# Performance work log

Measured on AMD Instinct MI355X. Metric: run time of the kernel, lower is better.

The kernel has to match this reference:

```python
import jax, jax.numpy as jnp
import numpy as np

B = 8          # batch of images
FH = FW = 28   # feature map size (layer2 of wide_resnet101_2 on 224x224)
IMG = 224      # input image H=W
C = 1024       # embedding dim (max of layer2/layer3 channels)
M = 50000      # coreset memory bank size
KS = 17        # GaussianBlur kernel size
SIGMA = 4.0


def _gauss_kernel():
    x = jnp.arange(KS, dtype=jnp.float32) - (KS - 1) / 2.0
    g = jnp.exp(-(x * x) / (2.0 * SIGMA * SIGMA))
    return g / jnp.sum(g)


def _gaussian_blur(masks):
    # masks: [B, H, W]; separable depthwise blur with reflect padding
    k = _gauss_kernel()
    pad = (KS - 1) // 2
    x = jnp.pad(masks, ((0, 0), (pad, pad), (pad, pad)), mode='reflect')[:, None]  # [B,1,H+2p,W+2p]
    x = jax.lax.conv_general_dilated(x, k[None, None, :, None], (1, 1), 'VALID',
                                     dimension_numbers=('NCHW', 'OIHW', 'NCHW'))
    x = jax.lax.conv_general_dilated(x, k[None, None, None, :], (1, 1), 'VALID',
                                     dimension_numbers=('NCHW', 'OIHW', 'NCHW'))
    return x[:, 0]


def setup_inputs() -> dict:
    key = jax.random.key(0)
    k1, k2 = jax.random.split(key)
    features = jax.random.normal(k1, (B * FH * FW, C), dtype=jnp.float32)
    memory = jax.random.normal(k2, (M, C), dtype=jnp.float32)
    return {"features": features, "memory": memory}


def reference(features, memory):
    # pairwise squared L2 distances via ||f||^2 + ||m||^2 - 2 f.m  -> [N, M]
    f2 = jnp.sum(features * features, axis=-1)            # [N]
    m2 = jnp.sum(memory * memory, axis=-1)                # [M]
    d2 = f2[:, None] + m2[None, :] - 2.0 * (features @ memory.T)
    score = jnp.sqrt(jnp.maximum(jnp.min(d2, axis=-1), 0.0))  # [N]
    image_scores = jnp.max(score.reshape(B, -1), axis=-1)     # [B]
    masks = score.reshape(B, FH, FW)
    # bilinear, align_corners=False == jax.image.resize 'linear' (half-pixel centers)
    masks = jax.image.resize(masks, (B, IMG, IMG), method='linear')
    masks = _gaussian_blur(masks)
    return image_scores, masks
```

## Files before the change

kernel.cpp:

```cpp
#include <hip/hip_runtime.h>
#include <hip/hip_bf16.h>
#include <float.h>

#define N_FEAT 6272
#define N_FPAD 6400
#define C_DIM  1024
#define M_MEM  50000
#define M_PAD  50176
#define B_IMG  8
#define IMGSZ  224
#define NTM    25
#define NTN    196
#define NT     4900

typedef __attribute__((ext_vector_type(8))) short bf16x8;
typedef __attribute__((ext_vector_type(4))) float f32x4;


__device__ inline unsigned short f2bf(float x) {
  unsigned int u = __float_as_uint(x);
  u += 0x7FFFu + ((u >> 16) & 1u);
  return (unsigned short)(u >> 16);
}

__global__ __launch_bounds__(256) void convert_rows_kernel(
    const float* __restrict__ src, unsigned short* __restrict__ dst,
    float* __restrict__ sq, unsigned int* __restrict__ minbits,
    int valid_rows, int total_rows)
{
  int row  = blockIdx.x * 4 + (threadIdx.x >> 6);
  int lane = threadIdx.x & 63;
  if (row >= total_rows) return;
  float s = 0.f;
  ushort4* d4 = (ushort4*)(dst + (size_t)row * C_DIM);
  if (row < valid_rows) {
    const float4* s4 = (const float4*)(src + (size_t)row * C_DIM);
    #pragma unroll
    for (int j = 0; j < 4; ++j) {
      float4 v = s4[lane + 64 * j];
      ushort4 o = make_ushort4(f2bf(v.x), f2bf(v.y), f2bf(v.z), f2bf(v.w));
      d4[lane + 64 * j] = o;
      s += v.x * v.x + v.y * v.y + v.z * v.z + v.w * v.w;
    }
  } else {
    ushort4 z = make_ushort4(0, 0, 0, 0);
    #pragma unroll
    for (int j = 0; j < 4; ++j) d4[lane + 64 * j] = z;
  }
  #pragma unroll
  for (int off = 32; off > 0; off >>= 1) s += __shfl_down(s, off, 64);
  if (lane == 0) {
    sq[row] = (row < valid_rows) ? s : FLT_MAX;
    if (minbits && row < valid_rows) minbits[row] = 0x7F7FFFFFu;
  }
}

__global__ __launch_bounds__(512, 2) void gemm_min_kernel(
    const unsigned short* __restrict__ A,
    const unsigned short* __restrict__ Bm,
    const float* __restrict__ f2, const float* __restrict__ m2,
    unsigned int* __restrict__ minbits)
{
  extern __shared__ char smem[];

  const int orig = blockIdx.x;
  const int xcd  = orig & 7;
  const int wg   = ((xcd < 4) ? xcd * 613 : 2452 + (xcd - 4) * 612) + (orig >> 3);
  const int g    = wg / 980;
  const int rem  = wg - g * 980;
  const int tileN = rem / 5;
  const int tileM = g * 5 + (rem - tileN * 5);

  const int tid  = threadIdx.x;
  const int w    = tid >> 6, lane = tid & 63;
  const int wr   = w >> 2, wc = w & 3;
  const int quad = lane >> 4, r16 = lane & 15;

  const unsigned short* gAp[2];
  const unsigned short* gBp[2];
  int offA[2], offB[2];
  {
    const int rowInBlk = lane >> 2;
    const int qsrc = (lane & 3) ^ ((lane >> 3) & 3);
    #pragma unroll
    for (int j = 0; j < 2; ++j) {
      const int m = w * 2 + j;
      const int row = m * 16 + rowInBlk;
      gAp[j] = A  + (size_t)(tileM * 256 + row) * C_DIM + qsrc * 8;
      gBp[j] = Bm + (size_t)(tileN * 256 + row) * C_DIM + qsrc * 8;
      offA[j] = m * 1024;
      offB[j] = 16384 + m * 1024;
    }
  }

  auto stage = [&](int kt) {
    char* sl = smem + ((kt & 3) << 15);
    const int ko = kt * 32;
    #pragma unroll
    for (int j = 0; j < 2; ++j) {
      __builtin_amdgcn_global_load_lds(
        (const __attribute__((address_space(1))) unsigned int*)(gAp[j] + ko),
        (__attribute__((address_space(3))) unsigned int*)(sl + offA[j]), 16, 0, 0);
      __builtin_amdgcn_global_load_lds(
        (const __attribute__((address_space(1))) unsigned int*)(gBp[j] + ko),
        (__attribute__((address_space(3))) unsigned int*)(sl + offB[j]), 16, 0, 0);
    }
  };

  f32x4 acc[8][4] = {};
  const int fsw   = quad ^ ((r16 >> 1) & 3);
  const int aBase = (wr * 128 + r16) * 4 + fsw;
  const int bBase = (wc * 64  + r16) * 4 + fsw;

  stage(0); stage(1); stage(2);

  auto body = [&](int kt, bool doStage) {
    __builtin_amdgcn_s_barrier();
    __builtin_amdgcn_sched_barrier(0);
    if (doStage) stage(kt + 3);
    const char* base = smem + ((kt & 3) << 15);
    const bf16x8* LA = (const bf16x8*)base;
    const bf16x8* LB = (const bf16x8*)(base + 16384);
    bf16x8 b[4], a[4];
    #pragma unroll
    for (int j = 0; j < 4; ++j) b[j] = LB[bBase + j * 64];
    #pragma unroll
    for (int i = 0; i < 4; ++i) a[i] = LA[aBase + i * 64];
    __builtin_amdgcn_s_setprio(1);
    #pragma unroll
    for (int i = 0; i < 4; ++i)
      #pragma unroll
      for (int j = 0; j < 4; ++j)
        acc[i][j] = __builtin_amdgcn_mfma_f32_16x16x32_bf16(a[i], b[j], acc[i][j], 0, 0, 0);
    __builtin_amdgcn_s_setprio(0);
    bf16x8 a2[4];
    #pragma unroll
    for (int i = 0; i < 4; ++i) a2[i] = LA[aBase + (i + 4) * 64];
    __builtin_amdgcn_s_barrier();
    __builtin_amdgcn_sched_barrier(0);
    __builtin_amdgcn_s_setprio(1);
    #pragma unroll
    for (int i = 0; i < 4; ++i)
      #pragma unroll
      for (int j = 0; j < 4; ++j)
        acc[i + 4][j] = __builtin_amdgcn_mfma_f32_16x16x32_bf16(a2[i], b[j], acc[i + 4][j], 0, 0, 0);
    __builtin_amdgcn_s_setprio(0);
  };

  for (int kt = 0; kt < 30; ++kt) {
    asm volatile("s_waitcnt vmcnt(8)" ::: "memory");
    body(kt, kt < 29);
  }
  asm volatile("s_waitcnt vmcnt(4)" ::: "memory");
  body(30, false);
  asm volatile("s_waitcnt vmcnt(0)" ::: "memory");
  body(31, false);

  const int colbase = tileN * 256 + wc * 64 + r16;
  float m2v[4];
  #pragma unroll
  for (int j = 0; j < 4; ++j) m2v[j] = m2[colbase + j * 16];
  const int rowq = tileM * 256 + wr * 128 + quad * 4;
  #pragma unroll
  for (int i = 0; i < 8; ++i) {
    #pragma unroll
    for (int r = 0; r < 4; ++r) {
      const int n = rowq + i * 16 + r;
      const float f2v = f2[n];
      float best = FLT_MAX;
      #pragma unroll
      for (int j = 0; j < 4; ++j) {
        float d = f2v + m2v[j] - 2.0f * acc[i][j][r];
        d = fmaxf(d, 0.0f);
        best = fminf(best, d);
      }
      best = fminf(best, __shfl_xor(best, 1, 64));
      best = fminf(best, __shfl_xor(best, 2, 64));
      best = fminf(best, __shfl_xor(best, 4, 64));
      best = fminf(best, __shfl_xor(best, 8, 64));
      if (r16 == 0) atomicMin(minbits + n, __float_as_uint(best));
    }
  }
}

__global__ __launch_bounds__(256) void finalize_kernel(
    const unsigned int* __restrict__ minbits, float* __restrict__ m28,
    float* __restrict__ image_scores)
{
  int b = blockIdx.x, tid = threadIdx.x;
  float mx = 0.f;
  for (int i = tid; i < 784; i += 256) {
    float s = sqrtf(__uint_as_float(minbits[b * 784 + i]));
    m28[b * 784 + i] = s;
    mx = fmaxf(mx, s);
  }
  #pragma unroll
  for (int off = 32; off > 0; off >>= 1) mx = fmaxf(mx, __shfl_down(mx, off, 64));
  __shared__ float red[4];
  if ((tid & 63) == 0) red[tid >> 6] = mx;
  __syncthreads();
  if (tid == 0) image_scores[b] = fmaxf(fmaxf(red[0], red[1]), fmaxf(red[2], red[3]));
}

__global__ __launch_bounds__(256) void resize_kernel(
    const float* __restrict__ m28, float* __restrict__ out)
{
  int idx = blockIdx.x * 256 + threadIdx.x;
  if (idx >= B_IMG * IMGSZ * IMGSZ) return;
  int x = idx % IMGSZ, y = (idx / IMGSZ) % IMGSZ, b = idx / (IMGSZ * IMGSZ);
  float sy = (y + 0.5f) * 0.125f - 0.5f;
  float sx = (x + 0.5f) * 0.125f - 0.5f;
  int iy0 = (int)floorf(sy); float fy = sy - (float)iy0;
  int ix0 = (int)floorf(sx); float fx = sx - (float)ix0;
  int y0 = min(max(iy0, 0), 27), y1 = min(max(iy0 + 1, 0), 27);
  int x0 = min(max(ix0, 0), 27), x1 = min(max(ix0 + 1, 0), 27);
  const float* p = m28 + b * 784;
  float v00 = p[y0 * 28 + x0], v01 = p[y0 * 28 + x1];
  float v10 = p[y1 * 28 + x0], v11 = p[y1 * 28 + x1];
  out[idx] = (1.f - fy) * ((1.f - fx) * v00 + fx * v01) +
             fy         * ((1.f - fx) * v10 + fx * v11);
}

__device__ inline void gauss17(float* g) {
  float s = 0.f;
  #pragma unroll
  for (int i = 0; i < 17; ++i) {
    float x = (float)(i - 8);
    g[i] = expf(-x * x * (1.0f / 32.0f));
    s += g[i];
  }
  float inv = 1.0f / s;
  #pragma unroll
  for (int i = 0; i < 17; ++i) g[i] *= inv;
}

__device__ inline int refl(int t) { return t < 0 ? -t : (t > 223 ? 446 - t : t); }

__global__ __launch_bounds__(256) void blur_h_kernel(
    const float* __restrict__ in, float* __restrict__ out)
{
  int idx = blockIdx.x * 256 + threadIdx.x;
  if (idx >= B_IMG * IMGSZ * IMGSZ) return;
  int x = idx % IMGSZ, y = (idx / IMGSZ) % IMGSZ, b = idx / (IMGSZ * IMGSZ);
  float g[17]; gauss17(g);
  const float* row = in + (size_t)b * IMGSZ * IMGSZ + y * IMGSZ;
  float s = 0.f;
  #pragma unroll
  for (int k = 0; k < 17; ++k) s += g[k] * row[refl(x + k - 8)];
  out[idx] = s;
}

__global__ __launch_bounds__(256) void blur_v_kernel(
    const float* __restrict__ in, float* __restrict__ out)
{
  int idx = blockIdx.x * 256 + threadIdx.x;
  if (idx >= B_IMG * IMGSZ * IMGSZ) return;
  int x = idx % IMGSZ, y = (idx / IMGSZ) % IMGSZ, b = idx / (IMGSZ * IMGSZ);
  float g[17]; gauss17(g);
  const float* img = in + (size_t)b * IMGSZ * IMGSZ;
  float s = 0.f;
  #pragma unroll
  for (int k = 0; k < 17; ++k) s += g[k] * img[refl(y + k - 8) * IMGSZ + x];
  out[idx] = s;
}

extern "C" void kernel_launch(void* const* d_in, const int* in_sizes, int n_in,
                              void* d_out, int out_size, void* d_ws, size_t ws_size,
                              hipStream_t stream) {
  const float* features = (const float*)d_in[0];
  const float* memory   = (const float*)d_in[1];
  if (n_in >= 2 && in_sizes[0] > in_sizes[1]) {
    const float* t = features; features = memory; memory = t;
  }
  float* out = (float*)d_out;
  char* ws = (char*)d_ws;

  unsigned short* memB  = (unsigned short*)(ws);
  unsigned short* featB = (unsigned short*)(ws + 102760448);
  float*        f2      = (float*)(ws + 115867648);
  float*        m2      = (float*)(ws + 115893248);
  unsigned int* minb    = (unsigned int*)(ws + 116093952);
  float*        m28     = (float*)(ws + 116119552);
  float*        rsz     = (float*)(ws);
  float*        tmp     = (float*)(ws + 1605632);

  static int attr_done = 0;
  if (!attr_done) {
    hipFuncSetAttribute((const void*)gemm_min_kernel,
                        hipFuncAttributeMaxDynamicSharedMemorySize, 131072);
    attr_done = 1;
  }

  convert_rows_kernel<<<M_PAD / 4, 256, 0, stream>>>(memory, memB, m2, nullptr, M_MEM, M_PAD);
  convert_rows_kernel<<<N_FPAD / 4, 256, 0, stream>>>(features, featB, f2, minb, N_FEAT, N_FPAD);

  gemm_min_kernel<<<NT, 512, 131072, stream>>>(featB, memB, f2, m2, minb);

  finalize_kernel<<<B_IMG, 256, 0, stream>>>(minb, m28, out);
  resize_kernel<<<(B_IMG * IMGSZ * IMGSZ) / 256, 256, 0, stream>>>(m28, rsz);
  blur_h_kernel<<<(B_IMG * IMGSZ * IMGSZ) / 256, 256, 0, stream>>>(rsz, tmp);
  blur_v_kernel<<<(B_IMG * IMGSZ * IMGSZ) / 256, 256, 0, stream>>>(tmp, out + 8);
}
```

Measured before the change: 1.097 ms.

## Restructure GEMM main loop to process two K-stages per iteration with finer barrier phases

Replaces the 4-slot, 3-ahead single-stage pipeline with a loop that consumes two K-stages (64 K-elements) per iteration from a double-buffered pair of LDS slots. The MFMAs are split into four phases separated by barriers, and the next stage loads are issued early and mid-iteration. The aim is to interleave LDS reads, global-to-LDS loads and MFMAs more finely and to halve loop/barrier overhead per K. In exchange, prefetch depth drops and there are more barriers per iteration, which risks exposing global-load latency or adding sync stalls.

```diff
diff --git a/kernel.cpp b/kernel.cpp
--- a/kernel.cpp
+++ b/kernel.cpp
@@ -16,6 +16,8 @@
 typedef __attribute__((ext_vector_type(8))) short bf16x8;
 typedef __attribute__((ext_vector_type(4))) float f32x4;
 
+#define MFMA16(a, b, c) __builtin_amdgcn_mfma_f32_16x16x32_bf16((a), (b), (c), 0, 0, 0)
+
 
 __device__ inline unsigned short f2bf(float x) {
   unsigned int u = __float_as_uint(x);
@@ -93,9 +95,9 @@
     }
   }
 
-  auto stage = [&](int kt) {
-    char* sl = smem + ((kt & 3) << 15);
-    const int ko = kt * 32;
+  auto stage = [&](int s) {
+    char* sl = smem + ((s & 3) << 15);
+    const int ko = s * 32;
     #pragma unroll
     for (int j = 0; j < 2; ++j) {
       __builtin_amdgcn_global_load_lds(
@@ -112,49 +114,65 @@
   const int aBase = (wr * 128 + r16) * 4 + fsw;
   const int bBase = (wc * 64  + r16) * 4 + fsw;
 
-  stage(0); stage(1); stage(2);
-
-  auto body = [&](int kt, bool doStage) {
+  stage(0); stage(1);
+
+  for (int t = 0; t < 16; ++t) {
+    const bool ds = (t < 15);
+    const char* base = smem + ((t & 1) << 16);
+    const bf16x8* LA0 = (const bf16x8*)(base);
+    const bf16x8* LB0 = (const bf16x8*)(base + 16384);
+    const bf16x8* LA1 = (const bf16x8*)(base + 32768);
+    const bf16x8* LB1 = (const bf16x8*)(base + 49152);
+    bf16x8 b0[4], b1[4];
+
+    if (ds) {
+      stage(2 * t + 2);
+      asm volatile("s_waitcnt vmcnt(4)" ::: "memory");
+    } else {
+      asm volatile("s_waitcnt vmcnt(0)" ::: "memory");
+    }
     __builtin_amdgcn_s_barrier();
     __builtin_amdgcn_sched_barrier(0);
-    if (doStage) stage(kt + 3);
-    const char* base = smem + ((kt & 3) << 15);
-    const bf16x8* LA = (const bf16x8*)base;
-    const bf16x8* LB = (const bf16x8*)(base + 16384);
-    bf16x8 b[4], a[4];
-    #pragma unroll
-    for (int j = 0; j < 4; ++j) b[j] = LB[bBase + j * 64];
-    #pragma unroll
-    for (int i = 0; i < 4; ++i) a[i] = LA[aBase + i * 64];
-    __builtin_amdgcn_s_setprio(1);
-    #pragma unroll
-    for (int i = 0; i < 4; ++i)
-      #pragma unroll
-      for (int j = 0; j < 4; ++j)
-        acc[i][j] = __builtin_amdgcn_mfma_f32_16x16x32_bf16(a[i], b[j], acc[i][j], 0, 0, 0);
-    __builtin_amdgcn_s_setprio(0);
-    bf16x8 a2[4];
-    #pragma unroll
-    for (int i = 0; i < 4; ++i) a2[i] = LA[aBase + (i + 4) * 64];
+    {
+      #pragma unroll
+      for (int j = 0; j < 4; ++j) b0[j] = LB0[bBase + j * 64];
+      bf16x8 x0 = LA0[aBase + 0 * 64], x1 = LA0[aBase + 1 * 64];
+      #pragma unroll
+      for (int j = 0; j < 4; ++j) b1[j] = LB1[bBase + j * 64];
+      bf16x8 y0 = LA1[aBase + 0 * 64], y1 = LA1[aBase + 1 * 64];
+      __builtin_amdgcn_s_setprio(1);
+      #pragma unroll
+      for (int j = 0; j < 4; ++j) {
+        acc[0][j] = MFMA16(x0, b0[j], acc[0][j]);
+        acc[1][j] = MFMA16(x1, b0[j], acc[1][j]);
+        acc[0][j] = MFMA16(y0, b1[j], acc[0][j]);
+        acc[1][j] = MFMA16(y1, b1[j], acc[1][j]);
+      }
+      __builtin_amdgcn_s_setprio(0);
+    }
     __builtin_amdgcn_s_barrier();
-    __builtin_amdgcn_sched_barrier(0);
-    __builtin_amdgcn_s_setprio(1);
-    #pragma unroll
-    for (int i = 0; i < 4; ++i)
-      #pragma unroll
-      for (int j = 0; j < 4; ++j)
-        acc[i + 4][j] = __builtin_amdgcn_mfma_f32_16x16x32_bf16(a2[i], b[j], acc[i + 4][j], 0, 0, 0);
-    __builtin_amdgcn_s_setprio(0);
-  };
-
-  for (int kt = 0; kt < 30; ++kt) {
-    asm volatile("s_waitcnt vmcnt(8)" ::: "memory");
-    body(kt, kt < 29);
-  }
-  asm volatile("s_waitcnt vmcnt(4)" ::: "memory");
-  body(30, false);
-  asm volatile("s_waitcnt vmcnt(0)" ::: "memory");
-  body(31, false);
+
+    #pragma unroll
+    for (int q = 1; q < 4; ++q) {
+      bf16x8 x0 = LA0[aBase + (2 * q) * 64], x1 = LA0[aBase + (2 * q + 1) * 64];
+      bf16x8 y0 = LA1[aBase + (2 * q) * 64], y1 = LA1[aBase + (2 * q + 1) * 64];
+      if (q == 2 && ds) stage(2 * t + 3);
+      __builtin_amdgcn_s_barrier();
+      __builtin_amdgcn_sched_barrier(0);
+      asm volatile("s_waitcnt lgkmcnt(0)" ::: "memory");
+      __builtin_amdgcn_sched_barrier(0);
+      __builtin_amdgcn_s_setprio(1);
+      #pragma unroll
+      for (int j = 0; j < 4; ++j) {
+        acc[2 * q][j]     = MFMA16(x0, b0[j], acc[2 * q][j]);
+        acc[2 * q + 1][j] = MFMA16(x1, b0[j], acc[2 * q + 1][j]);
+        acc[2 * q][j]     = MFMA16(y0, b1[j], acc[2 * q][j]);
+        acc[2 * q + 1][j] = MFMA16(y1, b1[j], acc[2 * q + 1][j]);
+      }
+      __builtin_amdgcn_s_setprio(0);
+      __builtin_amdgcn_s_barrier();
+    }
+  }
 
   const int colbase = tileN * 256 + wc * 64 + r16;
   float m2v[4];
```

Measured after the change: 1.173 ms. 7.0% more time.
